# Performance work log

Measured on AMD Instinct MI355X. Metric: run time of the kernel, lower is better.

Reference implementation:

```python
import jax, jax.numpy as jnp
import numpy as np

D = 2048
H = 16
DK = D // H
B = 2
S = 2048


def setup_inputs() -> dict:
    key = jax.random.key(0)
    ks = jax.random.split(key, 11)
    s = 1.0 / np.sqrt(D)
    inp = {
        "q": jax.random.normal(ks[0], (B, S, D), jnp.float32),
        "k": jax.random.normal(ks[1], (B, S, D), jnp.float32),
        "v": jax.random.normal(ks[2], (B, S, D), jnp.float32),
        "mask": 0,
        "Wq": jax.random.normal(ks[3], (D, D), jnp.float32) * s,
        "bq": jax.random.normal(ks[4], (D,), jnp.float32) * s,
        "Wk": jax.random.normal(ks[5], (D, D), jnp.float32) * s,
        "bk": jax.random.normal(ks[6], (D,), jnp.float32) * s,
        "Wv": jax.random.normal(ks[7], (D, D), jnp.float32) * s,
        "bv": jax.random.normal(ks[8], (D,), jnp.float32) * s,
        "Wo": jax.random.normal(ks[9], (D, D), jnp.float32) * s,
        "bo": jax.random.normal(ks[10], (D,), jnp.float32) * s,
    }
    return inp


def reference(q, k, v, mask, Wq, bq, Wk, bk, Wv, bv, Wo, bo):
    # Linear projections (torch Linear: x @ W.T + b)
    query = q @ Wq.T + bq  # [B,S,D]
    key_ = k @ Wk.T + bk
    value = v @ Wv.T + bv
    # split heads -> [B,S,H,DK]
    query = query.reshape(B, S, H, DK)
    key_ = key_.reshape(B, S, H, DK)
    value = value.reshape(B, S, H, DK)
    # scores [B,H,Sq,Sk]
    scores = jnp.einsum('nqhd,nkhd->nhqk', query, key_)
    if mask:
        # faithful to source: fill where triu(ones, diag=1) == 0 (lower tri incl diag)
        tri = jnp.triu(jnp.ones((S, S), jnp.float32), k=1)
        scores = jnp.where(tri == 0, jnp.float32(-1e20), scores)
    attn = jax.nn.softmax(scores / np.sqrt(DK), axis=3)
    # dropout=0.0 -> identity
    out = jnp.einsum('nhql,nlhd->nqhd', attn, value).reshape(B, S, D)
    return out @ Wo.T + bo
```

## Files before the change

### kernel.cpp

```cpp
#include <hip/hip_runtime.h>
#include <math.h>

typedef unsigned short u16;
typedef u16 u16x8 __attribute__((ext_vector_type(8)));
typedef u16 u16x4 __attribute__((ext_vector_type(4)));
typedef short s16x8 __attribute__((ext_vector_type(8)));
typedef short s16x4 __attribute__((ext_vector_type(4)));
typedef float f32x4 __attribute__((ext_vector_type(4)));

static constexpr int B_ = 2;
static constexpr int S_ = 2048;
static constexpr int D_ = 2048;
static constexpr int H_ = 16;
static constexpr int DK = 128;
static constexpr long long BSD = (long long)B_ * S_ * D_;
static constexpr long long DD  = (long long)D_ * D_;

#if __has_builtin(__builtin_amdgcn_mfma_f32_16x16x32_bf16)
#define HAVE_MFMA32 1
#else
#define HAVE_MFMA32 0
#endif
#if __has_builtin(__builtin_amdgcn_mfma_f32_16x16x16bf16_1k)
#define HAVE_MFMA16 1
#else
#define HAVE_MFMA16 0
#endif

__device__ __forceinline__ u16 f2bf(float f) {
    union { float f; unsigned u; } cv; cv.f = f;
    unsigned u = cv.u;
    return (u16)((u + 0x7fffu + ((u >> 16) & 1u)) >> 16);
}

__device__ __forceinline__ unsigned pack2bf(float a, float b) {
    union { float f; unsigned u; } x, y; x.f = a; y.f = b;
    return ((y.u + 0x8000u) & 0xffff0000u) | ((x.u + 0x8000u) >> 16);
}

__device__ __forceinline__ f32x4 mfma32(f32x4 c, u16x8 a, u16x8 b) {
#if HAVE_MFMA32
    return __builtin_amdgcn_mfma_f32_16x16x32_bf16((s16x8)a, (s16x8)b, c, 0, 0, 0);
#else
    asm volatile("v_mfma_f32_16x16x32_bf16 %0, %1, %2, %0" : "+v"(c) : "v"(a), "v"(b));
    return c;
#endif
}
__device__ __forceinline__ f32x4 mfma16(f32x4 c, u16x4 a, u16x4 b) {
#if HAVE_MFMA16
    return __builtin_amdgcn_mfma_f32_16x16x16bf16_1k((s16x4)a, (s16x4)b, c, 0, 0, 0);
#else
    asm volatile("v_mfma_f32_16x16x16_bf16 %0, %1, %2, %0" : "+v"(c) : "v"(a), "v"(b));
    return c;
#endif
}
__device__ __forceinline__ void fence32() {
#if !HAVE_MFMA32
    asm volatile("s_nop 7\ns_nop 7" :::);
#endif
}
__device__ __forceinline__ void fence16() {
#if !HAVE_MFMA16
    asm volatile("s_nop 7\ns_nop 7" :::);
#endif
}

__device__ __forceinline__ void glds16(const u16* g, u16* l) {
    __builtin_amdgcn_global_load_lds(
        (const __attribute__((address_space(1))) unsigned int*)g,
        (__attribute__((address_space(3))) unsigned int*)l, 16, 0, 0);
}

__device__ __forceinline__ float fexp2(float x) {
#if __has_builtin(__builtin_amdgcn_exp2f)
    return __builtin_amdgcn_exp2f(x);
#else
    return exp2f(x);
#endif
}

__global__ __launch_bounds__(256) void cast_f32_bf16(const float* __restrict__ x,
                                                     u16* __restrict__ y, int n4) {
    int i = blockIdx.x * 256 + threadIdx.x;
    if (i >= n4) return;
    float4 f = ((const float4*)x)[i];
    ushort4 o;
    o.x = f2bf(f.x); o.y = f2bf(f.y); o.z = f2bf(f.z); o.w = f2bf(f.w);
    ((ushort4*)y)[i] = o;
}

__global__ __launch_bounds__(256) void transpose_v(const u16* __restrict__ V,
                                                   u16* __restrict__ Vt) {
    __shared__ u16 tile[32][33];
    int z = blockIdx.z;
    int b = z >> 4, h = z & 15;
    const u16* src = V + (long long)b * S_ * D_ + (long long)h * DK;
    u16* dst = Vt + (long long)z * DK * S_;
    int l0 = blockIdx.x * 32, d0 = blockIdx.y * 32;
    int c = threadIdx.x & 31, r0 = threadIdx.x >> 5;
#pragma unroll
    for (int i = 0; i < 4; ++i) {
        int r = r0 + i * 8;
        tile[r][c] = src[(long long)(l0 + r) * D_ + d0 + c];
    }
    __syncthreads();
#pragma unroll
    for (int i = 0; i < 4; ++i) {
        int r = r0 + i * 8;
        dst[(long long)(d0 + r) * S_ + l0 + c] = tile[c][r];
    }
}

template <typename OutT, bool BIAS>
__global__ __launch_bounds__(256) void gemm_bt(const u16* __restrict__ A,
                                               const u16* __restrict__ B,
                                               OutT* __restrict__ C,
                                               const float* __restrict__ bias,
                                               float scale) {
    __shared__ u16 As[128 * 32];
    __shared__ u16 Bs[128 * 32];

    const int t = threadIdx.x;
    const int wave = t >> 6, lane = t & 63;
    const int quad = lane >> 4, l16 = lane & 15;
    const int wm = (wave >> 1) * 64;
    const int wn = (wave & 1) * 64;
    const long long m0 = (long long)blockIdx.y * 128;
    const long long n0 = (long long)blockIdx.x * 128;

    f32x4 acc[4][4];
#pragma unroll
    for (int i = 0; i < 4; ++i)
#pragma unroll
        for (int j = 0; j < 4; ++j)
            acc[i][j] = f32x4{0.f, 0.f, 0.f, 0.f};

    for (int k0 = 0; k0 < D_; k0 += 32) {
        __syncthreads();
#pragma unroll
        for (int s = 0; s < 2; ++s) {
            int slot = s * 256 + t;
            int row = slot >> 2;
            int c = (t & 3) ^ ((row >> 1) & 3);
            glds16(A + (m0 + row) * D_ + k0 + c * 8, &As[slot * 8]);
        }
#pragma unroll
        for (int s = 0; s < 2; ++s) {
            int slot = s * 256 + t;
            int row = slot >> 2;
            int c = (t & 3) ^ ((row >> 1) & 3);
            glds16(B + (n0 + row) * D_ + k0 + c * 8, &Bs[slot * 8]);
        }
        __syncthreads();

        u16x8 af[4], bf[4];
#pragma unroll
        for (int i = 0; i < 4; ++i) {
            int row = wm + i * 16 + l16;
            af[i] = *(const u16x8*)(&As[row * 32 + ((quad ^ ((row >> 1) & 3)) * 8)]);
        }
#pragma unroll
        for (int j = 0; j < 4; ++j) {
            int row = wn + j * 16 + l16;
            bf[j] = *(const u16x8*)(&Bs[row * 32 + ((quad ^ ((row >> 1) & 3)) * 8)]);
        }
#pragma unroll
        for (int i = 0; i < 4; ++i)
#pragma unroll
            for (int j = 0; j < 4; ++j)
                acc[i][j] = mfma32(acc[i][j], af[i], bf[j]);
    }

    fence32();

#pragma unroll
    for (int j = 0; j < 4; ++j) {
        int n = (int)n0 + wn + j * 16 + l16;
        float bs = BIAS ? bias[n] : 0.f;
#pragma unroll
        for (int i = 0; i < 4; ++i) {
            long long mbase = m0 + wm + i * 16 + quad * 4;
#pragma unroll
            for (int r = 0; r < 4; ++r) {
                float val = (acc[i][j][r] + bs) * scale;
                long long off = (mbase + r) * (long long)D_ + n;
                if constexpr (sizeof(OutT) == 4) C[off] = val;
                else                             C[off] = f2bf(val);
            }
        }
    }
}

__global__ __launch_bounds__(256, 2) void flash_attn(const u16* __restrict__ Qb,
                                                     const u16* __restrict__ Kb,
                                                     const u16* __restrict__ Vt,
                                                     u16* __restrict__ Ob) {
    const int qt = blockIdx.x;
    const int z  = blockIdx.y;
    const int b  = z >> 4, h = z & 15;
    const int t = threadIdx.x, wave = t >> 6, lane = t & 63;
    const int quad = lane >> 4, l16 = lane & 15;

    __shared__ u16 Ks[128 * 128];
    __shared__ u16 Vs[128 * 128];

    u16x8 qf[2][4];
    {
        const u16* qbase = Qb + ((long long)(b * S_ + qt * 128 + wave * 32 + l16)) * D_
                              + h * DK + quad * 8;
#pragma unroll
        for (int jq = 0; jq < 2; ++jq)
#pragma unroll
            for (int kk = 0; kk < 4; ++kk)
                qf[jq][kk] = *(const u16x8*)(qbase + (long long)jq * 16 * D_ + kk * 32);
    }

    f32x4 acc_o[2][8];
#pragma unroll
    for (int jq = 0; jq < 2; ++jq)
#pragma unroll
        for (int jd = 0; jd < 8; ++jd)
            acc_o[jq][jd] = f32x4{0.f, 0.f, 0.f, 0.f};
    float m_[2] = {-3e38f, -3e38f}, l_[2] = {0.f, 0.f};

    const u16* kbase = Kb + ((long long)(b * S_)) * D_ + h * DK;
    const u16* vbase = Vt + ((long long)z * DK) * S_;

    for (int kt = 0; kt < S_ / 128; ++kt) {
        __syncthreads();
        {
            const u16* ksrc = kbase + (long long)kt * 128 * D_;
#pragma unroll
            for (int i = 0; i < 8; ++i) {
                int s = i * 256 + t;
                int row = s >> 4;
                int c = (s & 15) ^ (row & 7);
                glds16(ksrc + (long long)row * D_ + c * 8, &Ks[s * 8]);
            }
        }
        {
            const u16* vsrc = vbase + kt * 128;
#pragma unroll
            for (int i = 0; i < 8; ++i) {
                int row = i * 16 + (t >> 4);
                int c = t & 15;
                u16x8 vv = *(const u16x8*)(vsrc + (long long)row * S_ + c * 8);
                u16x8 sw = __builtin_shufflevector(vv, vv, 4, 5, 6, 7, 0, 1, 2, 3);
                vv = (row & 1) ? sw : vv;
                *(u16x8*)(&Vs[row * 128 + ((c ^ ((row >> 1) & 7)) * 8)]) = vv;
            }
        }
        __syncthreads();

        f32x4 st[8][2];
#pragma unroll
        for (int ik = 0; ik < 8; ++ik)
#pragma unroll
            for (int jq = 0; jq < 2; ++jq)
                st[ik][jq] = f32x4{0.f, 0.f, 0.f, 0.f};
#pragma unroll
        for (int kk = 0; kk < 4; ++kk) {
            u16x8 kf[8];
#pragma unroll
            for (int ik = 0; ik < 8; ++ik) {
                int krow = ik * 16 + l16;
                kf[ik] = *(const u16x8*)(&Ks[krow * 128 + (((kk * 4 + quad) ^ (krow & 7)) * 8)]);
            }
#pragma unroll
            for (int ik = 0; ik < 8; ++ik) {
                st[ik][0] = mfma32(st[ik][0], kf[ik], qf[0][kk]);
                st[ik][1] = mfma32(st[ik][1], kf[ik], qf[1][kk]);
            }
        }
        fence32();

        float alpha[2];
#pragma unroll
        for (int jq = 0; jq < 2; ++jq) {
            float mx = st[0][jq][0];
#pragma unroll
            for (int ik = 0; ik < 8; ++ik)
#pragma unroll
                for (int r = 0; r < 4; ++r) mx = fmaxf(mx, st[ik][jq][r]);
            mx = fmaxf(mx, __shfl_xor(mx, 16, 64));
            mx = fmaxf(mx, __shfl_xor(mx, 32, 64));
            float mn = fmaxf(m_[jq], mx);
            alpha[jq] = fexp2(m_[jq] - mn);
            m_[jq] = mn;
            float sum = 0.f;
#pragma unroll
            for (int ik = 0; ik < 8; ++ik)
#pragma unroll
                for (int r = 0; r < 4; ++r) {
                    float p = fexp2(st[ik][jq][r] - mn);
                    st[ik][jq][r] = p;
                    sum += p;
                }
            sum += __shfl_xor(sum, 16, 64);
            sum += __shfl_xor(sum, 32, 64);
            l_[jq] = l_[jq] * alpha[jq] + sum;
        }

        float ar[2][4];
#pragma unroll
        for (int jq = 0; jq < 2; ++jq)
#pragma unroll
            for (int r = 0; r < 4; ++r)
                ar[jq][r] = __shfl(alpha[jq], quad * 20 + r, 64);
#pragma unroll
        for (int jq = 0; jq < 2; ++jq)
#pragma unroll
            for (int jd = 0; jd < 8; ++jd)
#pragma unroll
                for (int r = 0; r < 4; ++r)
                    acc_o[jq][jd][r] *= ar[jq][r];

#pragma unroll
        for (int ik = 0; ik < 8; ++ik) {
            u16x4 pf0, pf1;
            {
                union { u16x4 v; unsigned u[2]; } pk;
                pk.u[0] = pack2bf(st[ik][0][0], st[ik][0][1]);
                pk.u[1] = pack2bf(st[ik][0][2], st[ik][0][3]);
                pf0 = pk.v;
                pk.u[0] = pack2bf(st[ik][1][0], st[ik][1][1]);
                pk.u[1] = pack2bf(st[ik][1][2], st[ik][1][3]);
                pf1 = pk.v;
            }
            u16x4 vf[8];
#pragma unroll
            for (int jd = 0; jd < 8; ++jd) {
                int vrow = jd * 16 + l16;
                vf[jd] = *(const u16x4*)(&Vs[vrow * 128 + (((ik * 4 + quad) ^ l16) * 4)]);
            }
#pragma unroll
            for (int jd = 0; jd < 8; ++jd) {
                acc_o[0][jd] = mfma16(acc_o[0][jd], pf0, vf[jd]);
                acc_o[1][jd] = mfma16(acc_o[1][jd], pf1, vf[jd]);
            }
        }
        fence16();
    }

    float lr[2][4];
#pragma unroll
    for (int jq = 0; jq < 2; ++jq) {
        float inv = 1.f / l_[jq];
#pragma unroll
        for (int r = 0; r < 4; ++r)
            lr[jq][r] = __shfl(inv, quad * 20 + r, 64);
    }
    u16* obase = Ob + ((long long)(b * S_ + qt * 128 + wave * 32)) * D_ + h * DK;
#pragma unroll
    for (int jq = 0; jq < 2; ++jq)
#pragma unroll
        for (int r = 0; r < 4; ++r) {
            long long rowoff = (long long)(jq * 16 + quad * 4 + r) * D_;
#pragma unroll
            for (int jd = 0; jd < 8; ++jd)
                obase[rowoff + jd * 16 + l16] = f2bf(acc_o[jq][jd][r] * lr[jq][r]);
        }
}

extern "C" void kernel_launch(void* const* d_in, const int* in_sizes, int n_in,
                              void* d_out, int out_size, void* d_ws, size_t ws_size,
                              hipStream_t stream) {
    const float* q  = (const float*)d_in[0];
    const float* k  = (const float*)d_in[1];
    const float* v  = (const float*)d_in[2];
    const float* Wq = (const float*)d_in[4];
    const float* bq = (const float*)d_in[5];
    const float* Wk = (const float*)d_in[6];
    const float* bk = (const float*)d_in[7];
    const float* Wv = (const float*)d_in[8];
    const float* bv = (const float*)d_in[9];
    const float* Wo = (const float*)d_in[10];
    const float* bo = (const float*)d_in[11];
    float* out = (float*)d_out;

    u16* ws = (u16*)d_ws;
    u16* xq  = ws; ws += BSD;
    u16* xk  = ws; ws += BSD;
    u16* xv  = ws; ws += BSD;
    u16* wqb = ws; ws += DD;
    u16* wkb = ws; ws += DD;
    u16* wvb = ws; ws += DD;
    u16* wob = ws; ws += DD;
    u16* Qb  = ws; ws += BSD;
    u16* Kb  = ws; ws += BSD;
    u16* Vb  = ws; ws += BSD;
    u16* Vt  = ws; ws += BSD;
    u16* Ob  = ws; ws += BSD;

    const float q_scale = (float)(0.08838834764831845 * 1.4426950408889634);

    {
        int n4i = (int)(BSD / 4);
        cast_f32_bf16<<<n4i / 256, 256, 0, stream>>>(q, xq, n4i);
        cast_f32_bf16<<<n4i / 256, 256, 0, stream>>>(k, xk, n4i);
        cast_f32_bf16<<<n4i / 256, 256, 0, stream>>>(v, xv, n4i);
        int n4w = (int)(DD / 4);
        cast_f32_bf16<<<n4w / 256, 256, 0, stream>>>(Wq, wqb, n4w);
        cast_f32_bf16<<<n4w / 256, 256, 0, stream>>>(Wk, wkb, n4w);
        cast_f32_bf16<<<n4w / 256, 256, 0, stream>>>(Wv, wvb, n4w);
        cast_f32_bf16<<<n4w / 256, 256, 0, stream>>>(Wo, wob, n4w);
    }

    {
        dim3 g(D_ / 128, (B_ * S_) / 128);
        gemm_bt<u16, true><<<g, 256, 0, stream>>>(xq, wqb, Qb, bq, q_scale);
        gemm_bt<u16, true><<<g, 256, 0, stream>>>(xk, wkb, Kb, bk, 1.0f);
        gemm_bt<u16, true><<<g, 256, 0, stream>>>(xv, wvb, Vb, bv, 1.0f);
    }

    transpose_v<<<dim3(S_ / 32, DK / 32, B_ * H_), 256, 0, stream>>>(Vb, Vt);

    flash_attn<<<dim3(S_ / 128, B_ * H_), 256, 0, stream>>>(Qb, Kb, Vt, Ob);

    {
        dim3 g(D_ / 128, (B_ * S_) / 128);
        gemm_bt<float, true><<<g, 256, 0, stream>>>(Ob, wob, out, bo, 1.0f);
    }
}
```

Baseline: 497.5 us.

## Double-buffer flash attention with 512 threads, fuse casts, stage GEMM epilogue via LDS

Flash attention now runs 512-thread blocks covering 256 queries. K and V tiles are double-buffered in 128KB of dynamic LDS and loaded asynchronously with global_load_lds, so loads overlap compute and the per-tile second barrier is removed. The V-tile swizzle changes to match the direct LDS load, and the grid order is swapped. The output tiles of both the attention and the GEMMs are staged through LDS so global stores are vectorized and coalesced, and the seven cast kernels are merged into one launch. The risks are lower occupancy from 128KB of LDS and extra barriers in the epilogues.

```diff
diff --git a/kernel.cpp b/kernel.cpp
--- a/kernel.cpp
+++ b/kernel.cpp
@@ -79,14 +79,22 @@
 #endif
 }
 
-__global__ __launch_bounds__(256) void cast_f32_bf16(const float* __restrict__ x,
-                                                     u16* __restrict__ y, int n4) {
-    int i = blockIdx.x * 256 + threadIdx.x;
-    if (i >= n4) return;
-    float4 f = ((const float4*)x)[i];
+struct CastArgs {
+    const float* src[7];
+    u16* dst[7];
+    int start[8];
+};
+__global__ __launch_bounds__(256) void cast_all(CastArgs a) {
+    int g = blockIdx.x * 256 + threadIdx.x;
+    if (g >= a.start[7]) return;
+    int seg = 0;
+#pragma unroll
+    for (int i = 1; i < 7; ++i) seg += (g >= a.start[i]) ? 1 : 0;
+    int idx = g - a.start[seg];
+    float4 f = ((const float4*)a.src[seg])[idx];
     ushort4 o;
     o.x = f2bf(f.x); o.y = f2bf(f.y); o.z = f2bf(f.z); o.w = f2bf(f.w);
-    ((ushort4*)y)[i] = o;
+    ((ushort4*)a.dst[seg])[idx] = o;
 }
 
 __global__ __launch_bounds__(256) void transpose_v(const u16* __restrict__ V,
@@ -117,8 +125,9 @@
                                                OutT* __restrict__ C,
                                                const float* __restrict__ bias,
                                                float scale) {
-    __shared__ u16 As[128 * 32];
-    __shared__ u16 Bs[128 * 32];
+    __shared__ u16 SM[8192];
+    u16* As = SM;
+    u16* Bs = SM + 4096;
 
     const int t = threadIdx.x;
     const int wave = t >> 6, lane = t & 63;
@@ -173,40 +182,86 @@
 
     fence32();
 
-#pragma unroll
-    for (int j = 0; j < 4; ++j) {
-        int n = (int)n0 + wn + j * 16 + l16;
-        float bs = BIAS ? bias[n] : 0.f;
-#pragma unroll
-        for (int i = 0; i < 4; ++i) {
-            long long mbase = m0 + wm + i * 16 + quad * 4;
-#pragma unroll
-            for (int r = 0; r < 4; ++r) {
-                float val = (acc[i][j][r] + bs) * scale;
-                long long off = (mbase + r) * (long long)D_ + n;
-                if constexpr (sizeof(OutT) == 4) C[off] = val;
-                else                             C[off] = f2bf(val);
-            }
-        }
-    }
-}
-
-__global__ __launch_bounds__(256, 2) void flash_attn(const u16* __restrict__ Qb,
+    float bs[4];
+#pragma unroll
+    for (int j = 0; j < 4; ++j)
+        bs[j] = BIAS ? bias[(int)n0 + wn + j * 16 + l16] : 0.f;
+
+    if constexpr (sizeof(OutT) == 2) {
+#pragma unroll
+        for (int p = 0; p < 2; ++p) {
+            __syncthreads();
+#pragma unroll
+            for (int jj = 0; jj < 2; ++jj) {
+                int j = p * 2 + jj;
+#pragma unroll
+                for (int i = 0; i < 4; ++i)
+#pragma unroll
+                    for (int r = 0; r < 4; ++r) {
+                        int row = wm + i * 16 + quad * 4 + r;
+                        int lc = (wave & 1) * 32 + jj * 16 + l16;
+                        SM[row * 64 + lc] = f2bf((acc[i][j][r] + bs[j]) * scale);
+                    }
+            }
+            __syncthreads();
+#pragma unroll
+            for (int i = 0; i < 4; ++i) {
+                int idx = i * 256 + t;
+                int row = idx >> 3, cc = idx & 7;
+                u16x8 val = *(const u16x8*)(&SM[row * 64 + cc * 8]);
+                long long n = n0 + 32 * p + (cc & 3) * 8 + (cc >> 2) * 64;
+                *(u16x8*)((u16*)C + (m0 + row) * (long long)D_ + n) = val;
+            }
+        }
+    } else {
+        float* Cf = (float*)SM;
+#pragma unroll
+        for (int p = 0; p < 4; ++p) {
+            __syncthreads();
+            int j = p;
+#pragma unroll
+            for (int i = 0; i < 4; ++i)
+#pragma unroll
+                for (int r = 0; r < 4; ++r) {
+                    int row = wm + i * 16 + quad * 4 + r;
+                    int lc = (wave & 1) * 16 + l16;
+                    Cf[row * 32 + lc] = (acc[i][j][r] + bs[j]) * scale;
+                }
+            __syncthreads();
+#pragma unroll
+            for (int i = 0; i < 4; ++i) {
+                int idx = i * 256 + t;
+                int row = idx >> 3, cc = idx & 7;
+                f32x4 val = *(const f32x4*)(&Cf[row * 32 + cc * 4]);
+                long long n = n0 + 16 * p + (cc & 3) * 4 + (cc >> 2) * 64;
+                *(f32x4*)((float*)C + (m0 + row) * (long long)D_ + n) = val;
+            }
+        }
+    }
+}
+
+__global__ __launch_bounds__(512, 2) void flash_attn(const u16* __restrict__ Qb,
                                                      const u16* __restrict__ Kb,
                                                      const u16* __restrict__ Vt,
                                                      u16* __restrict__ Ob) {
-    const int qt = blockIdx.x;
-    const int z  = blockIdx.y;
+    extern __shared__ u16 SM[];
+    const int z  = blockIdx.x;
+    const int qt = blockIdx.y;
     const int b  = z >> 4, h = z & 15;
     const int t = threadIdx.x, wave = t >> 6, lane = t & 63;
     const int quad = lane >> 4, l16 = lane & 15;
 
-    __shared__ u16 Ks[128 * 128];
-    __shared__ u16 Vs[128 * 128];
+    u16* Ksb0 = SM;
+    u16* Ksb1 = SM + 16384;
+    u16* Vsb0 = SM + 32768;
+    u16* Vsb1 = SM + 49152;
+
+    const u16* kbase = Kb + (long long)(b * S_) * D_ + h * DK;
+    const u16* vbase = Vt + (long long)z * DK * S_;
 
     u16x8 qf[2][4];
     {
-        const u16* qbase = Qb + ((long long)(b * S_ + qt * 128 + wave * 32 + l16)) * D_
+        const u16* qbase = Qb + ((long long)(b * S_ + qt * 256 + wave * 32 + l16)) * D_
                               + h * DK + quad * 8;
 #pragma unroll
         for (int jq = 0; jq < 2; ++jq)
@@ -223,34 +278,48 @@
             acc_o[jq][jd] = f32x4{0.f, 0.f, 0.f, 0.f};
     float m_[2] = {-3e38f, -3e38f}, l_[2] = {0.f, 0.f};
 
-    const u16* kbase = Kb + ((long long)(b * S_)) * D_ + h * DK;
-    const u16* vbase = Vt + ((long long)z * DK) * S_;
+    {
+#pragma unroll
+        for (int i = 0; i < 4; ++i) {
+            int slot = i * 512 + t;
+            int row = slot >> 4;
+            int cs = (slot & 15) ^ (row & 7);
+            glds16(kbase + (long long)row * D_ + cs * 8, Ksb0 + slot * 8);
+        }
+#pragma unroll
+        for (int i = 0; i < 4; ++i) {
+            int slot = i * 512 + t;
+            int row = slot >> 4;
+            int cs = (slot & 15) ^ (row & 7);
+            glds16(vbase + (long long)row * S_ + cs * 8, Vsb0 + slot * 8);
+        }
+    }
 
     for (int kt = 0; kt < S_ / 128; ++kt) {
         __syncthreads();
-        {
-            const u16* ksrc = kbase + (long long)kt * 128 * D_;
-#pragma unroll
-            for (int i = 0; i < 8; ++i) {
-                int s = i * 256 + t;
-                int row = s >> 4;
-                int c = (s & 15) ^ (row & 7);
-                glds16(ksrc + (long long)row * D_ + c * 8, &Ks[s * 8]);
-            }
-        }
-        {
-            const u16* vsrc = vbase + kt * 128;
-#pragma unroll
-            for (int i = 0; i < 8; ++i) {
-                int row = i * 16 + (t >> 4);
-                int c = t & 15;
-                u16x8 vv = *(const u16x8*)(vsrc + (long long)row * S_ + c * 8);
-                u16x8 sw = __builtin_shufflevector(vv, vv, 4, 5, 6, 7, 0, 1, 2, 3);
-                vv = (row & 1) ? sw : vv;
-                *(u16x8*)(&Vs[row * 128 + ((c ^ ((row >> 1) & 7)) * 8)]) = vv;
-            }
-        }
-        __syncthreads();
+        const int p = kt & 1;
+        const u16* ks = p ? Ksb1 : Ksb0;
+        const u16* vs = p ? Vsb1 : Vsb0;
+        if (kt + 1 < S_ / 128) {
+            u16* kd = p ? Ksb0 : Ksb1;
+            u16* vd = p ? Vsb0 : Vsb1;
+            const u16* ksrc = kbase + (long long)(kt + 1) * 128 * D_;
+            const u16* vsrc = vbase + (kt + 1) * 128;
+#pragma unroll
+            for (int i = 0; i < 4; ++i) {
+                int slot = i * 512 + t;
+                int row = slot >> 4;
+                int cs = (slot & 15) ^ (row & 7);
+                glds16(ksrc + (long long)row * D_ + cs * 8, kd + slot * 8);
+            }
+#pragma unroll
+            for (int i = 0; i < 4; ++i) {
+                int slot = i * 512 + t;
+                int row = slot >> 4;
+                int cs = (slot & 15) ^ (row & 7);
+                glds16(vsrc + (long long)row * S_ + cs * 8, vd + slot * 8);
+            }
+        }
 
         f32x4 st[8][2];
 #pragma unroll
@@ -264,7 +333,7 @@
 #pragma unroll
             for (int ik = 0; ik < 8; ++ik) {
                 int krow = ik * 16 + l16;
-                kf[ik] = *(const u16x8*)(&Ks[krow * 128 + (((kk * 4 + quad) ^ (krow & 7)) * 8)]);
+                kf[ik] = *(const u16x8*)(&ks[krow * 128 + (((kk * 4 + quad) ^ (l16 & 7)) * 8)]);
             }
 #pragma unroll
             for (int ik = 0; ik < 8; ++ik) {
@@ -292,9 +361,9 @@
             for (int ik = 0; ik < 8; ++ik)
 #pragma unroll
                 for (int r = 0; r < 4; ++r) {
-                    float p = fexp2(st[ik][jq][r] - mn);
-                    st[ik][jq][r] = p;
-                    sum += p;
+                    float pv = fexp2(st[ik][jq][r] - mn);
+                    st[ik][jq][r] = pv;
+                    sum += pv;
                 }
             sum += __shfl_xor(sum, 16, 64);
             sum += __shfl_xor(sum, 32, 64);
@@ -327,11 +396,13 @@
                 pk.u[1] = pack2bf(st[ik][1][2], st[ik][1][3]);
                 pf1 = pk.v;
             }
+            const int kc = ik * 4 + quad;
+            const int chi = kc >> 1, clo = kc & 1;
             u16x4 vf[8];
 #pragma unroll
             for (int jd = 0; jd < 8; ++jd) {
                 int vrow = jd * 16 + l16;
-                vf[jd] = *(const u16x4*)(&Vs[vrow * 128 + (((ik * 4 + quad) ^ l16) * 4)]);
+                vf[jd] = *(const u16x4*)(&vs[vrow * 128 + ((chi ^ (l16 & 7)) * 8) + clo * 4]);
             }
 #pragma unroll
             for (int jd = 0; jd < 8; ++jd) {
@@ -350,16 +421,24 @@
         for (int r = 0; r < 4; ++r)
             lr[jq][r] = __shfl(inv, quad * 20 + r, 64);
     }
-    u16* obase = Ob + ((long long)(b * S_ + qt * 128 + wave * 32)) * D_ + h * DK;
+    __syncthreads();
 #pragma unroll
     for (int jq = 0; jq < 2; ++jq)
 #pragma unroll
         for (int r = 0; r < 4; ++r) {
-            long long rowoff = (long long)(jq * 16 + quad * 4 + r) * D_;
+            int qloc = wave * 32 + jq * 16 + quad * 4 + r;
 #pragma unroll
             for (int jd = 0; jd < 8; ++jd)
-                obase[rowoff + jd * 16 + l16] = f2bf(acc_o[jq][jd][r] * lr[jq][r]);
-        }
+                SM[qloc * 128 + jd * 16 + l16] = f2bf(acc_o[jq][jd][r] * lr[jq][r]);
+        }
+    __syncthreads();
+    u16* obase = Ob + ((long long)(b * S_ + qt * 256)) * D_ + h * DK;
+#pragma unroll
+    for (int i = 0; i < 8; ++i) {
+        int idx = i * 512 + t;
+        int row = idx >> 4, cc = idx & 15;
+        *(u16x8*)(obase + (long long)row * D_ + cc * 8) = *(const u16x8*)(&SM[row * 128 + cc * 8]);
+    }
 }
 
 extern "C" void kernel_launch(void* const* d_in, const int* in_sizes, int n_in,
@@ -395,15 +474,15 @@
     const float q_scale = (float)(0.08838834764831845 * 1.4426950408889634);
 
     {
-        int n4i = (int)(BSD / 4);
-        cast_f32_bf16<<<n4i / 256, 256, 0, stream>>>(q, xq, n4i);
-        cast_f32_bf16<<<n4i / 256, 256, 0, stream>>>(k, xk, n4i);
-        cast_f32_bf16<<<n4i / 256, 256, 0, stream>>>(v, xv, n4i);
-        int n4w = (int)(DD / 4);
-        cast_f32_bf16<<<n4w / 256, 256, 0, stream>>>(Wq, wqb, n4w);
-        cast_f32_bf16<<<n4w / 256, 256, 0, stream>>>(Wk, wkb, n4w);
-        cast_f32_bf16<<<n4w / 256, 256, 0, stream>>>(Wv, wvb, n4w);
-        cast_f32_bf16<<<n4w / 256, 256, 0, stream>>>(Wo, wob, n4w);
+        CastArgs a;
+        const float* srcs[7] = {q, k, v, Wq, Wk, Wv, Wo};
+        u16* dsts[7] = {xq, xk, xv, wqb, wkb, wvb, wob};
+        int n4s[7] = {(int)(BSD / 4), (int)(BSD / 4), (int)(BSD / 4),
+                      (int)(DD / 4), (int)(DD / 4), (int)(DD / 4), (int)(DD / 4)};
+        int acc = 0;
+        for (int i = 0; i < 7; ++i) { a.src[i] = srcs[i]; a.dst[i] = dsts[i]; a.start[i] = acc; acc += n4s[i]; }
+        a.start[7] = acc;
+        cast_all<<<(acc + 255) / 256, 256, 0, stream>>>(a);
     }
 
     {
@@ -415,7 +494,9 @@
 
     transpose_v<<<dim3(S_ / 32, DK / 32, B_ * H_), 256, 0, stream>>>(Vb, Vt);
 
-    flash_attn<<<dim3(S_ / 128, B_ * H_), 256, 0, stream>>>(Qb, Kb, Vt, Ob);
+    hipFuncSetAttribute((const void*)flash_attn,
+                        hipFuncAttributeMaxDynamicSharedMemorySize, 131072);
+    flash_attn<<<dim3(B_ * H_, S_ / 256), 512, 131072, stream>>>(Qb, Kb, Vt, Ob);
 
     {
         dim3 g(D_ / 128, (B_ * S_) / 128);
```

After: 474.2 us. 1.05x faster.
